# Optimization experiments

Measured on AMD Instinct MI355X. Metric: run time of the kernel, lower is better.

The kernel has to match this reference:

```python
import jax, jax.numpy as jnp
import numpy as np

B, SQ, SK, D, H = 2, 2048, 2048, 1024, 16
DK = D // H


def setup_inputs() -> dict:
    key = jax.random.key(0)
    ks = jax.random.split(key, 16)
    s = 1.0 / np.sqrt(D)
    inp = {
        "query": jax.random.normal(ks[0], (B, SQ, D), jnp.float32),
        "key": jax.random.normal(ks[1], (B, SK, D), jnp.float32),
        "value": jax.random.normal(ks[2], (B, SK, D), jnp.float32),
        "R": jax.random.normal(ks[3], (B, SK, D), jnp.float32),
        "Wq": jax.random.normal(ks[4], (D, D), jnp.float32) * s,
        "bq": jnp.zeros((D,), jnp.float32),
        "Wv": jax.random.normal(ks[5], (D, D), jnp.float32) * s,
        "bv": jnp.zeros((D,), jnp.float32),
        "Wr": jax.random.normal(ks[6], (D, D), jnp.float32) * s,
        "br": jnp.zeros((D,), jnp.float32),
        "W_h": jax.random.normal(ks[7], (H, DK, DK), jnp.float32) * (1.0 / np.sqrt(DK)),
        "Wo": jax.random.normal(ks[8], (D, D), jnp.float32) * s,
        "bo": jnp.zeros((D,), jnp.float32),
    }
    return inp


def _forward(query, key, value, R, Wq, bq, Wv, bv, Wr, br, W_h, Wo, bo):
    scale = 1.0 / np.sqrt(DK)
    # projections (torch Linear: x @ W.T + b)
    Q = (query @ Wq.T + bq).reshape(B, SQ, H, DK).transpose(0, 2, 1, 3)   # (B,H,SQ,DK)
    V = (value @ Wv.T + bv).reshape(B, SK, H, DK).transpose(0, 2, 1, 3)   # (B,H,SK,DK)
    Rp = (R @ Wr.T + br).reshape(B, SK, H, DK).transpose(0, 2, 1, 3)      # (B,H,SK,DK)
    # torch einsum 'hnk,bhn->bhn' sums W_h over its last axis -> elementwise gate
    w_rowsum = W_h.sum(axis=-1)  # (H, DK)

    def step(h, r_t):
        h_new = jnp.tanh(h * w_rowsum + r_t)  # (B,H,DK)
        return h_new, h_new

    h0 = jnp.zeros((B, H, DK), Rp.dtype)
    Rt = Rp.transpose(2, 0, 1, 3)  # (SK,B,H,DK)
    _, Hs = jax.lax.scan(step, h0, Rt)
    Hst = Hs.transpose(1, 2, 0, 3)  # (B,H,SK,DK)

    scores = jnp.einsum('bhqd,bhkd->bhqk', Q, Hst) * scale
    attn = jax.nn.softmax(scores, axis=-1)
    out = jnp.einsum('bhqk,bhkd->bhqd', attn, V)
    out = out.transpose(0, 2, 1, 3).reshape(B, SQ, D)
    return out @ Wo.T + bo


def reference(query, key, value, R, Wq, bq, Wv, bv, Wr, br, W_h, Wo, bo):
    return _forward(query, key, value, R, Wq, bq, Wv, bv, Wr, br, W_h, Wo, bo)
```

## Files before the change

### kernel.cpp

```cpp
#include <hip/hip_runtime.h>
#include <stdint.h>

typedef unsigned short u16;
typedef __attribute__((ext_vector_type(8))) _Float16 h8;
typedef __attribute__((ext_vector_type(2))) __fp16 hp2;
typedef __attribute__((ext_vector_type(4))) float f4;

#define B_ 2
#define SQ_ 2048
#define SK_ 2048
#define D_ 1024
#define H_ 16
#define DK_ 64

#define C_PROG  0
#define CTRL_N  512

__device__ __forceinline__ u16 f2h(float f) {
  union { _Float16 h; u16 u; } v; v.h = (_Float16)f; return v.u;
}
__device__ __forceinline__ unsigned pkrtz(float a, float b) {
  union { hp2 h; unsigned u; } v; v.h = __builtin_amdgcn_cvt_pkrtz(a, b); return v.u;
}
__device__ __forceinline__ float fexp2(float x) {
  float r;
  asm("v_exp_f32 %0, %1" : "=v"(r) : "v"(x));
  return r;
}

typedef const void __attribute__((address_space(1)))* gas1;
typedef void __attribute__((address_space(3)))* las3;
__device__ __forceinline__ void gld16(const void* g, void* l) {
  __builtin_amdgcn_global_load_lds((gas1)g, (las3)l, 16, 0, 0);
}

__device__ __forceinline__ void spin_ge(int* p, int v) {
  if (__hip_atomic_load(p, __ATOMIC_RELAXED, __HIP_MEMORY_SCOPE_AGENT) >= v) return;
  int n = 0;
  for (;;) {
    __builtin_amdgcn_s_sleep(16);
    int x = ((++n & 63) == 0)
                ? __hip_atomic_load(p, __ATOMIC_ACQUIRE, __HIP_MEMORY_SCOPE_AGENT)
                : __hip_atomic_load(p, __ATOMIC_RELAXED, __HIP_MEMORY_SCOPE_AGENT);
    if (x >= v) return;
    if (n > 8192) return;
  }
}

__device__ __forceinline__ void cast8(const float* __restrict__ src,
                                      u16* __restrict__ dst, int i) {
  float4 a = *(const float4*)(src + i);
  float4 b = *(const float4*)(src + i + 4);
  alignas(16) u16 t[8] = {f2h(a.x), f2h(a.y), f2h(a.z), f2h(a.w),
                          f2h(b.x), f2h(b.y), f2h(b.z), f2h(b.w)};
  *(int4*)(dst + i) = *(int4*)t;
}

__global__ void rma_cast_all(const float* __restrict__ xq, const float* __restrict__ xv,
                             const float* __restrict__ xr, const float* __restrict__ wq,
                             const float* __restrict__ wv, const float* __restrict__ wr,
                             const float* __restrict__ wo, u16* __restrict__ oxq,
                             u16* __restrict__ oxv, u16* __restrict__ oxr,
                             u16* __restrict__ owq, u16* __restrict__ owv,
                             u16* __restrict__ owr, u16* __restrict__ owo,
                             int* __restrict__ ctrl) {
  const int b = blockIdx.x;
  if (b == 0) { ctrl[threadIdx.x] = 0; ctrl[256 + threadIdx.x] = 0; }
  const float* src; u16* dst; int bi;
  if (b < 2048)      { src = xq; dst = oxq; bi = b; }
  else if (b < 4096) { src = xv; dst = oxv; bi = b - 2048; }
  else if (b < 6144) { src = xr; dst = oxr; bi = b - 4096; }
  else if (b < 6656) { src = wq; dst = owq; bi = b - 6144; }
  else if (b < 7168) { src = wv; dst = owv; bi = b - 6656; }
  else if (b < 7680) { src = wr; dst = owr; bi = b - 7168; }
  else               { src = wo; dst = owo; bi = b - 7680; }
  cast8(src, dst, (bi * 256 + threadIdx.x) * 8);
}

__device__ __forceinline__ void gemm_mainloop(
    const u16* __restrict__ A, const u16* __restrict__ Bw, int K,
    u16* As, u16* Bs, int m0, int n0, f4 (&acc)[4][4]) {
  const int tid = threadIdx.x;
  const int w = tid >> 6, lane = tid & 63;
  const int quad = lane >> 4, ln = lane & 15;
  const int wm = (w >> 1) * 64, wn = (w & 1) * 64;
  const int c0 = tid, c1 = tid + 256;
  const u16* a0 = A + (size_t)(m0 + (c0 >> 2)) * K + (c0 & 3) * 8;
  const u16* a1 = A + (size_t)(m0 + (c1 >> 2)) * K + (c1 & 3) * 8;
  const u16* b0 = Bw + (size_t)(n0 + (c0 >> 2)) * K + (c0 & 3) * 8;
  const u16* b1 = Bw + (size_t)(n0 + (c1 >> 2)) * K + (c1 & 3) * 8;
  u16* As0 = As + (0 + w * 64) * 8;
  u16* As1 = As + (256 + w * 64) * 8;
  u16* Bs0 = Bs + (0 + w * 64) * 8;
  u16* Bs1 = Bs + (256 + w * 64) * 8;
  for (int kt = 0; kt < K; kt += 32) {
    gld16(a0 + kt, As0);
    gld16(a1 + kt, As1);
    gld16(b0 + kt, Bs0);
    gld16(b1 + kt, Bs1);
    __syncthreads();
    h8 af[4], bf[4];
#pragma unroll
    for (int i = 0; i < 4; i++)
      af[i] = *(const h8*)&As[(wm + i * 16 + ln) * 32 + quad * 8];
#pragma unroll
    for (int i = 0; i < 4; i++)
      bf[i] = *(const h8*)&Bs[(wn + i * 16 + ln) * 32 + quad * 8];
#pragma unroll
    for (int i = 0; i < 4; i++)
#pragma unroll
      for (int j = 0; j < 4; j++)
        acc[i][j] = __builtin_amdgcn_mfma_f32_16x16x32_f16(af[i], bf[j], acc[i][j], 0, 0, 0);
    __syncthreads();
  }
}

__device__ __forceinline__ void gemm_mainloop64(
    const u16* __restrict__ A, const u16* __restrict__ Bw, int K,
    u16* As, u16* Bs, int m0, int n0, f4 (&acc)[2][4]) {
  const int tid = threadIdx.x;
  const int w = tid >> 6, lane = tid & 63;
  const int quad = lane >> 4, ln = lane & 15;
  const int wm = (w >> 1) * 32, wn = (w & 1) * 64;
  const u16* a0 = A + (size_t)(m0 + (tid >> 2)) * K + (tid & 3) * 8;
  const u16* b0 = Bw + (size_t)(n0 + (tid >> 2)) * K + (tid & 3) * 8;
  const u16* b1 = Bw + (size_t)(n0 + ((tid + 256) >> 2)) * K + (tid & 3) * 8;
  u16* As0 = As + (w * 64) * 8;
  u16* Bs0 = Bs + (w * 64) * 8;
  u16* Bs1 = Bs + (256 + w * 64) * 8;
  for (int kt = 0; kt < K; kt += 32) {
    gld16(a0 + kt, As0);
    gld16(b0 + kt, Bs0);
    gld16(b1 + kt, Bs1);
    __syncthreads();
    h8 af[2], bf[4];
#pragma unroll
    for (int i = 0; i < 2; i++)
      af[i] = *(const h8*)&As[(wm + i * 16 + ln) * 32 + quad * 8];
#pragma unroll
    for (int j = 0; j < 4; j++)
      bf[j] = *(const h8*)&Bs[(wn + j * 16 + ln) * 32 + quad * 8];
#pragma unroll
    for (int i = 0; i < 2; i++)
#pragma unroll
      for (int j = 0; j < 4; j++)
        acc[i][j] = __builtin_amdgcn_mfma_f32_16x16x32_f16(af[i], bf[j], acc[i][j], 0, 0, 0);
    __syncthreads();
  }
}

__global__ __launch_bounds__(256, 2)
void rma_proj_gemm(const u16* __restrict__ Xq, const u16* __restrict__ Xv,
                   const u16* __restrict__ Xr, const u16* __restrict__ Wq,
                   const u16* __restrict__ Wv, const u16* __restrict__ Wr,
                   const float* __restrict__ bq, const float* __restrict__ bv,
                   const float* __restrict__ br, u16* __restrict__ Qb,
                   u16* __restrict__ Vt, float* __restrict__ Rp) {
  const int z = blockIdx.z;
  const u16* A = z == 0 ? Xq : (z == 1 ? Xv : Xr);
  const u16* Bw = z == 0 ? Wq : (z == 1 ? Wv : Wr);
  const float* bias = z == 0 ? bq : (z == 1 ? bv : br);
  __shared__ u16 As[128 * 32];
  __shared__ u16 Bs[128 * 32];
  const int m0 = blockIdx.x * 128, n0 = blockIdx.y * 128;
  f4 acc[4][4] = {};
  gemm_mainloop(A, Bw, D_, As, Bs, m0, n0, acc);
  const int tid = threadIdx.x;
  const int w = tid >> 6, lane = tid & 63;
  const int quad = lane >> 4, ln = lane & 15;
  const int wm = (w >> 1) * 64, wn = (w & 1) * 64;
#pragma unroll
  for (int i = 0; i < 4; i++)
#pragma unroll
    for (int j = 0; j < 4; j++) {
      const int colg = n0 + wn + j * 16 + ln;
      const float bb = bias[colg];
      const int h = colg >> 6, d = colg & 63;
      const int row4 = m0 + wm + i * 16 + quad * 4;
      const int b = row4 >> 11, s = row4 & 2047;
      if (z == 1) {
        uint2 pk;
        pk.x = pkrtz(acc[i][j][0] + bb, acc[i][j][1] + bb);
        pk.y = pkrtz(acc[i][j][2] + bb, acc[i][j][3] + bb);
        *(uint2*)&Vt[((size_t)((b * H_ + h) * DK_ + d)) * SK_ + s] = pk;
      } else {
#pragma unroll
        for (int r = 0; r < 4; r++) {
          const float v = acc[i][j][r] + bb;
          const size_t idx = ((size_t)(b * H_ + h) * SK_ + (s + r)) * DK_ + d;
          if (z == 2) Rp[idx] = v;
          else Qb[idx] = f2h(v);
        }
      }
    }
}

#define RB_ 32
__device__ void recur_run(const float* __restrict__ Rp, const float* __restrict__ Wh,
                          u16* __restrict__ Hst, int* ctrl) {
  __builtin_amdgcn_s_setprio(2);
  const int tid = threadIdx.x;
  const int ch = blockIdx.x * 256 + tid;
  const int bh = ch >> 6, d = ch & 63, h = bh & 15;
  const float* wr = Wh + (h * 64 + d) * 64;
  float ws = 0.f;
#pragma unroll
  for (int k = 0; k < 64; k += 4) {
    float4 wv4 = *(const float4*)(wr + k);
    ws += (wv4.x + wv4.y) + (wv4.z + wv4.w);
  }
  const float C2 = 2.885390081777927f;
  const float wsC2 = ws * C2;
  const float Kw = 2.0f * wsC2;
  const size_t base = (size_t)bh * (SK_ * DK_) + d;
  const float* r = Rp + base;
  u16* o = Hst + base;
  int* pg = ctrl + C_PROG + bh * 16;
  float cur[RB_], nxt[RB_];
#pragma unroll
  for (int j = 0; j < RB_; j++) cur[j] = r[(size_t)j * DK_];
  float e = fexp2(cur[0] * C2);
  for (int t0 = 0; t0 < SK_; t0 += RB_) {
    const int t1 = t0 + RB_;
    const int tn = (t1 < SK_) ? t1 : t0;
#pragma unroll
    for (int j = 0; j < RB_; j++) nxt[j] = r[(size_t)(tn + j) * DK_];
#pragma unroll
    for (int j = 0; j < RB_; j++) {
      const float a = e + 1.0f;
      const float bb = __builtin_amdgcn_rcpf(a);
      const float hs = __builtin_fmaf(-2.0f, bb, 1.0f);
      o[(size_t)(t0 + j) * DK_] = f2h(hs);
      const float rn = (j + 1 < RB_) ? cur[j + 1] : nxt[0];
      const float K = __builtin_fmaf(C2, rn, wsC2);
      const float x = __builtin_fmaf(-Kw, bb, K);
      e = fexp2(x);
    }
    if (((t1 & 127) == 0) && (tid & 63) == 0)
      __hip_atomic_store(pg, t1, __ATOMIC_RELEASE, __HIP_MEMORY_SCOPE_AGENT);
#pragma unroll
    for (int j = 0; j < RB_; j++) cur[j] = nxt[j];
  }
  __builtin_amdgcn_s_setprio(0);
}

#define FXM_ 12.0f
__device__ void flash_task(int fidx, const u16* __restrict__ Qb,
                           const u16* __restrict__ Hst, const u16* __restrict__ Vt,
                           u16* __restrict__ Og, u16* smem, int* ctrl) {
  const int tid = threadIdx.x;
  const int w = tid >> 6, lane = tid & 63;
  const int quad = lane >> 4, ln = lane & 15;
  const int bh = fidx >> 4, qtile = fidx & 15;
  const int q0 = qtile * 128 + w * 32;
  u16* Kt = smem;
  u16* Vts = smem + 64 * 72;
  u16* Pw = smem + 2 * 64 * 72 + w * (32 * 72);
  const float scale2 = 0.18033688011112042f;
  const u16* Qg = Qb + (size_t)bh * SQ_ * DK_;
  const u16* Kg = Hst + (size_t)bh * SK_ * DK_;
  const u16* Vg = Vt + (size_t)bh * DK_ * SK_;
  int* pg = ctrl + C_PROG + bh * 16;
  if (tid == 0) spin_ge(pg, 128);
  __syncthreads();
  h8 qf[2][2];
#pragma unroll
  for (int qt = 0; qt < 2; qt++)
#pragma unroll
    for (int c = 0; c < 2; c++)
      qf[qt][c] = *(const h8*)&Qg[(size_t)(q0 + qt * 16 + ln) * DK_ + c * 32 + quad * 8];
  f4 o[4][2] = {};
  float l[2] = {0.f, 0.f};
  const int c0 = tid, c1 = tid + 256;
  const int r0 = c0 >> 3, o0 = (c0 & 7) * 8;
  const int r1 = c1 >> 3, o1 = (c1 & 7) * 8;
  const u16* kg0 = Kg + (size_t)r0 * DK_ + o0;
  const u16* kg1 = Kg + (size_t)r1 * DK_ + o1;
  const u16* vg0 = Vg + (size_t)r0 * SK_ + o0;
  const u16* vg1 = Vg + (size_t)r1 * SK_ + o1;
  u16* kl0 = &Kt[r0 * 72 + o0];
  u16* kl1 = &Kt[r1 * 72 + o1];
  u16* vl0 = &Vts[r0 * 72 + o0];
  u16* vl1 = &Vts[r1 * 72 + o1];
  int4 ks0 = *(const int4*)(kg0);
  int4 ks1 = *(const int4*)(kg1);
  int4 vs0 = *(const int4*)(vg0);
  int4 vs1 = *(const int4*)(vg1);
  int seen = 128;
  for (int kt = 0; kt < SK_; kt += 64) {
    if (tid == 0) {
      const int need = (kt + 128 <= SK_) ? kt + 128 : SK_;
      if (seen < need) { spin_ge(pg, need); seen = need; }
    }
    __syncthreads();
    *(int4*)kl0 = ks0;
    *(int4*)kl1 = ks1;
    *(int4*)vl0 = vs0;
    *(int4*)vl1 = vs1;
    __syncthreads();
    h8 kf[4][2], vf[4][2];
#pragma unroll
    for (int m = 0; m < 4; m++) {
      kf[m][0] = *(const h8*)&Kt[(m * 16 + ln) * 72 + quad * 8];
      kf[m][1] = *(const h8*)&Kt[(m * 16 + ln) * 72 + 32 + quad * 8];
    }
#pragma unroll
    for (int dt = 0; dt < 4; dt++) {
      vf[dt][0] = *(const h8*)&Vts[(dt * 16 + ln) * 72 + quad * 8];
      vf[dt][1] = *(const h8*)&Vts[(dt * 16 + ln) * 72 + 32 + quad * 8];
    }
    const int ktn = (kt + 64 < SK_) ? kt + 64 : 0;
    ks0 = *(const int4*)(kg0 + (size_t)ktn * DK_);
    ks1 = *(const int4*)(kg1 + (size_t)ktn * DK_);
    vs0 = *(const int4*)(vg0 + ktn);
    vs1 = *(const int4*)(vg1 + ktn);
    f4 st[4][2];
#pragma unroll
    for (int m = 0; m < 4; m++)
#pragma unroll
      for (int qt = 0; qt < 2; qt++) {
        f4 t = {0.f, 0.f, 0.f, 0.f};
        t = __builtin_amdgcn_mfma_f32_16x16x32_f16(kf[m][0], qf[qt][0], t, 0, 0, 0);
        t = __builtin_amdgcn_mfma_f32_16x16x32_f16(kf[m][1], qf[qt][1], t, 0, 0, 0);
        st[m][qt] = t;
      }
#pragma unroll
    for (int qt = 0; qt < 2; qt++)
#pragma unroll
      for (int m = 0; m < 4; m++) {
        const float p0 = fexp2(__builtin_fmaf(st[m][qt][0], scale2, -FXM_));
        const float p1 = fexp2(__builtin_fmaf(st[m][qt][1], scale2, -FXM_));
        const float p2 = fexp2(__builtin_fmaf(st[m][qt][2], scale2, -FXM_));
        const float p3 = fexp2(__builtin_fmaf(st[m][qt][3], scale2, -FXM_));
        l[qt] += (p0 + p1) + (p2 + p3);
        uint2 pk;
        pk.x = pkrtz(p0, p1);
        pk.y = pkrtz(p2, p3);
        *(uint2*)&Pw[(qt * 16 + ln) * 72 + m * 16 + quad * 4] = pk;
      }
    asm volatile("" ::: "memory");
#pragma unroll
    for (int c = 0; c < 2; c++) {
      h8 pb0 = *(const h8*)&Pw[(0 + ln) * 72 + c * 32 + quad * 8];
      h8 pb1 = *(const h8*)&Pw[(16 + ln) * 72 + c * 32 + quad * 8];
#pragma unroll
      for (int dt = 0; dt < 4; dt++) {
        o[dt][0] = __builtin_amdgcn_mfma_f32_16x16x32_f16(vf[dt][c], pb0, o[dt][0], 0, 0, 0);
        o[dt][1] = __builtin_amdgcn_mfma_f32_16x16x32_f16(vf[dt][c], pb1, o[dt][1], 0, 0, 0);
      }
    }
  }
  const int b = bh >> 4, h = bh & 15;
#pragma unroll
  for (int qt = 0; qt < 2; qt++) {
    float lq = l[qt];
    lq += __shfl_xor(lq, 16);
    lq += __shfl_xor(lq, 32);
    const float linv = __builtin_amdgcn_rcpf(lq);
    const int q = q0 + qt * 16 + ln;
#pragma unroll
    for (int dt = 0; dt < 4; dt++) {
      uint2 pk;
      pk.x = pkrtz(o[dt][qt][0] * linv, o[dt][qt][1] * linv);
      pk.y = pkrtz(o[dt][qt][2] * linv, o[dt][qt][3] * linv);
      *(uint2*)&Og[((size_t)b * SQ_ + q) * D_ + h * DK_ + dt * 16 + quad * 4] = pk;
    }
  }
}

__global__ __launch_bounds__(256, 2)
void rma_recur_flash(const float* __restrict__ Rp, const float* __restrict__ Wh,
                     u16* __restrict__ Hst, const u16* __restrict__ Qb,
                     const u16* __restrict__ Vt, u16* __restrict__ Og,
                     int* __restrict__ ctrl) {
  __shared__ __align__(16) u16 smem[18432];
  if (blockIdx.x < 8) {
    recur_run(Rp, Wh, Hst, ctrl);
    return;
  }
  flash_task(blockIdx.x - 8, Qb, Hst, Vt, Og, smem, ctrl);
}

__global__ __launch_bounds__(256, 2)
void rma_final_gemm(const u16* __restrict__ Og, const u16* __restrict__ Wo,
                    const float* __restrict__ bo, float* __restrict__ out) {
  __shared__ u16 As[64 * 32];
  __shared__ u16 Bs[128 * 32];
  const int m0 = blockIdx.x * 64, n0 = blockIdx.y * 128;
  f4 acc[2][4] = {};
  gemm_mainloop64(Og, Wo, D_, As, Bs, m0, n0, acc);
  const int tid = threadIdx.x;
  const int w = tid >> 6, lane = tid & 63;
  const int quad = lane >> 4, ln = lane & 15;
  const int wm = (w >> 1) * 32, wn = (w & 1) * 64;
#pragma unroll
  for (int i = 0; i < 2; i++)
#pragma unroll
    for (int j = 0; j < 4; j++) {
      const int colg = n0 + wn + j * 16 + ln;
      const float bb = bo[colg];
#pragma unroll
      for (int r = 0; r < 4; r++) {
        const int rowg = m0 + wm + i * 16 + quad * 4 + r;
        out[(size_t)rowg * D_ + colg] = acc[i][j][r] + bb;
      }
    }
}

extern "C" void kernel_launch(void* const* d_in, const int* in_sizes, int n_in,
                              void* d_out, int out_size, void* d_ws, size_t ws_size,
                              hipStream_t stream) {
  const float* query = (const float*)d_in[0];
  const float* value = (const float*)d_in[2];
  const float* R = (const float*)d_in[3];
  const float* Wq = (const float*)d_in[4];
  const float* bq = (const float*)d_in[5];
  const float* Wv = (const float*)d_in[6];
  const float* bv = (const float*)d_in[7];
  const float* Wr = (const float*)d_in[8];
  const float* br = (const float*)d_in[9];
  const float* W_h = (const float*)d_in[10];
  const float* Wo = (const float*)d_in[11];
  const float* bo = (const float*)d_in[12];
  float* out = (float*)d_out;

  char* ws = (char*)d_ws;
  const size_t MB = 1 << 20;
  u16* Xq = (u16*)(ws + 0 * MB);
  u16* Xv = (u16*)(ws + 8 * MB);
  u16* Xr = (u16*)(ws + 16 * MB);
  u16* Wqb = (u16*)(ws + 24 * MB);
  u16* Wvb = (u16*)(ws + 26 * MB);
  u16* Wrb = (u16*)(ws + 28 * MB);
  u16* Wob = (u16*)(ws + 30 * MB);
  u16* Qb = (u16*)(ws + 32 * MB);
  u16* Vt = (u16*)(ws + 40 * MB);
  float* Rp = (float*)(ws + 48 * MB);
  u16* Hs = (u16*)(ws + 64 * MB);
  u16* Og = (u16*)(ws + 72 * MB);
  int* ctrl = (int*)(ws + 80 * MB);

  rma_cast_all<<<dim3(8192), 256, 0, stream>>>(query, value, R, Wq, Wv, Wr, Wo,
                                               Xq, Xv, Xr, Wqb, Wvb, Wrb, Wob, ctrl);
  rma_proj_gemm<<<dim3(32, 8, 3), 256, 0, stream>>>(Xq, Xv, Xr, Wqb, Wvb, Wrb,
                                                    bq, bv, br, Qb, Vt, Rp);
  rma_recur_flash<<<dim3(520), 256, 0, stream>>>(Rp, W_h, Hs, Qb, Vt, Og, ctrl);
  rma_final_gemm<<<dim3(64, 8), 256, 0, stream>>>(Og, Wob, bo, out);
}
```

Measured before the change: 286.0 us.

## Fuse cast, projections, recurrence, attention and output GEMM into one persistent kernel

Merges the four launches (cast, projection GEMM, recurrence+flash, output GEMM) into a single persistent 520-block kernel coordinated by global atomic counters. The R path is cast and projected first, and the recurrence waits on per-row-tile counters, so it can start before the Q/V projections finish. The output GEMM starts per tile once the matching attention tiles are done. This removes kernel-launch boundaries and lets the serial recurrence overlap the rest, but it relies on all blocks being co-resident and on spin-waits with a timeout fallback, which risks deadlock or reading incomplete data. Launch bounds are raised to 4 blocks per CU.

```diff
diff --git a/kernel.cpp b/kernel.cpp
--- a/kernel.cpp
+++ b/kernel.cpp
@@ -13,8 +13,13 @@
 #define H_ 16
 #define DK_ 64
 
-#define C_PROG  0
-#define CTRL_N  512
+#define C_CASTRW 0
+#define C_CAST   4
+#define C_PROJ   8
+#define C_RDONE  32
+#define C_PROG   64
+#define C_OG     576
+#define CTRL_N   1088
 
 __device__ __forceinline__ u16 f2h(float f) {
   union { _Float16 h; u16 u; } v; v.h = (_Float16)f; return v.u;
@@ -43,8 +48,15 @@
                 ? __hip_atomic_load(p, __ATOMIC_ACQUIRE, __HIP_MEMORY_SCOPE_AGENT)
                 : __hip_atomic_load(p, __ATOMIC_RELAXED, __HIP_MEMORY_SCOPE_AGENT);
     if (x >= v) return;
-    if (n > 8192) return;
-  }
+    if (n > 16384) return;
+  }
+}
+__device__ __forceinline__ void rel_add(int* p, int v) {
+  __hip_atomic_fetch_add(p, v, __ATOMIC_RELEASE, __HIP_MEMORY_SCOPE_AGENT);
+}
+
+__global__ void rma_init(int* __restrict__ ctrl) {
+  for (int k = threadIdx.x; k < CTRL_N; k += 256) ctrl[k] = 0;
 }
 
 __device__ __forceinline__ void cast8(const float* __restrict__ src,
@@ -56,25 +68,23 @@
   *(int4*)(dst + i) = *(int4*)t;
 }
 
-__global__ void rma_cast_all(const float* __restrict__ xq, const float* __restrict__ xv,
-                             const float* __restrict__ xr, const float* __restrict__ wq,
-                             const float* __restrict__ wv, const float* __restrict__ wr,
-                             const float* __restrict__ wo, u16* __restrict__ oxq,
-                             u16* __restrict__ oxv, u16* __restrict__ oxr,
-                             u16* __restrict__ owq, u16* __restrict__ owv,
-                             u16* __restrict__ owr, u16* __restrict__ owo,
-                             int* __restrict__ ctrl) {
-  const int b = blockIdx.x;
-  if (b == 0) { ctrl[threadIdx.x] = 0; ctrl[256 + threadIdx.x] = 0; }
-  const float* src; u16* dst; int bi;
-  if (b < 2048)      { src = xq; dst = oxq; bi = b; }
-  else if (b < 4096) { src = xv; dst = oxv; bi = b - 2048; }
-  else if (b < 6144) { src = xr; dst = oxr; bi = b - 4096; }
-  else if (b < 6656) { src = wq; dst = owq; bi = b - 6144; }
-  else if (b < 7168) { src = wv; dst = owv; bi = b - 6656; }
-  else if (b < 7680) { src = wr; dst = owr; bi = b - 7168; }
-  else               { src = wo; dst = owo; bi = b - 7680; }
-  cast8(src, dst, (bi * 256 + threadIdx.x) * 8);
+__device__ __forceinline__ void cast_unit(
+    int u, int tid, const float* __restrict__ q, const float* __restrict__ v,
+    const float* __restrict__ r, const float* __restrict__ wq,
+    const float* __restrict__ wv, const float* __restrict__ wr,
+    const float* __restrict__ wo, u16* __restrict__ xq, u16* __restrict__ xv,
+    u16* __restrict__ xr, u16* __restrict__ owq, u16* __restrict__ owv,
+    u16* __restrict__ owr, u16* __restrict__ owo) {
+  const float* src; u16* dst; int off;
+  if (u < 256)      { src = r;  dst = xr;  off = u << 14; }
+  else if (u < 320) { src = wr; dst = owr; off = (u - 256) << 14; }
+  else if (u < 576) { src = q;  dst = xq;  off = (u - 320) << 14; }
+  else if (u < 832) { src = v;  dst = xv;  off = (u - 576) << 14; }
+  else if (u < 896) { src = wq; dst = owq; off = (u - 832) << 14; }
+  else if (u < 960) { src = wv; dst = owv; off = (u - 896) << 14; }
+  else              { src = wo; dst = owo; off = (u - 960) << 14; }
+#pragma unroll
+  for (int it = 0; it < 8; it++) cast8(src, dst, off + it * 2048 + tid * 8);
 }
 
 __device__ __forceinline__ void gemm_mainloop(
@@ -149,59 +159,13 @@
   }
 }
 
-__global__ __launch_bounds__(256, 2)
-void rma_proj_gemm(const u16* __restrict__ Xq, const u16* __restrict__ Xv,
-                   const u16* __restrict__ Xr, const u16* __restrict__ Wq,
-                   const u16* __restrict__ Wv, const u16* __restrict__ Wr,
-                   const float* __restrict__ bq, const float* __restrict__ bv,
-                   const float* __restrict__ br, u16* __restrict__ Qb,
-                   u16* __restrict__ Vt, float* __restrict__ Rp) {
-  const int z = blockIdx.z;
-  const u16* A = z == 0 ? Xq : (z == 1 ? Xv : Xr);
-  const u16* Bw = z == 0 ? Wq : (z == 1 ? Wv : Wr);
-  const float* bias = z == 0 ? bq : (z == 1 ? bv : br);
-  __shared__ u16 As[128 * 32];
-  __shared__ u16 Bs[128 * 32];
-  const int m0 = blockIdx.x * 128, n0 = blockIdx.y * 128;
-  f4 acc[4][4] = {};
-  gemm_mainloop(A, Bw, D_, As, Bs, m0, n0, acc);
-  const int tid = threadIdx.x;
-  const int w = tid >> 6, lane = tid & 63;
-  const int quad = lane >> 4, ln = lane & 15;
-  const int wm = (w >> 1) * 64, wn = (w & 1) * 64;
-#pragma unroll
-  for (int i = 0; i < 4; i++)
-#pragma unroll
-    for (int j = 0; j < 4; j++) {
-      const int colg = n0 + wn + j * 16 + ln;
-      const float bb = bias[colg];
-      const int h = colg >> 6, d = colg & 63;
-      const int row4 = m0 + wm + i * 16 + quad * 4;
-      const int b = row4 >> 11, s = row4 & 2047;
-      if (z == 1) {
-        uint2 pk;
-        pk.x = pkrtz(acc[i][j][0] + bb, acc[i][j][1] + bb);
-        pk.y = pkrtz(acc[i][j][2] + bb, acc[i][j][3] + bb);
-        *(uint2*)&Vt[((size_t)((b * H_ + h) * DK_ + d)) * SK_ + s] = pk;
-      } else {
-#pragma unroll
-        for (int r = 0; r < 4; r++) {
-          const float v = acc[i][j][r] + bb;
-          const size_t idx = ((size_t)(b * H_ + h) * SK_ + (s + r)) * DK_ + d;
-          if (z == 2) Rp[idx] = v;
-          else Qb[idx] = f2h(v);
-        }
-      }
-    }
-}
-
 #define RB_ 32
 __device__ void recur_run(const float* __restrict__ Rp, const float* __restrict__ Wh,
                           u16* __restrict__ Hst, int* ctrl) {
   __builtin_amdgcn_s_setprio(2);
   const int tid = threadIdx.x;
   const int ch = blockIdx.x * 256 + tid;
-  const int bh = ch >> 6, d = ch & 63, h = bh & 15;
+  const int bh = ch >> 6, d = ch & 63, h = bh & 15, b = bh >> 4;
   const float* wr = Wh + (h * 64 + d) * 64;
   float ws = 0.f;
 #pragma unroll
@@ -215,13 +179,16 @@
   const size_t base = (size_t)bh * (SK_ * DK_) + d;
   const float* r = Rp + base;
   u16* o = Hst + base;
+  int* rd = ctrl + C_RDONE + b * 16;
   int* pg = ctrl + C_PROG + bh * 16;
+  spin_ge(&rd[0], 8);
   float cur[RB_], nxt[RB_];
 #pragma unroll
   for (int j = 0; j < RB_; j++) cur[j] = r[(size_t)j * DK_];
   float e = fexp2(cur[0] * C2);
   for (int t0 = 0; t0 < SK_; t0 += RB_) {
     const int t1 = t0 + RB_;
+    if (t1 < SK_ && ((t1 & 127) == 0)) spin_ge(&rd[t1 >> 7], 8);
     const int tn = (t1 < SK_) ? t1 : t0;
 #pragma unroll
     for (int j = 0; j < RB_; j++) nxt[j] = r[(size_t)(tn + j) * DK_];
@@ -261,7 +228,7 @@
   const u16* Kg = Hst + (size_t)bh * SK_ * DK_;
   const u16* Vg = Vt + (size_t)bh * DK_ * SK_;
   int* pg = ctrl + C_PROG + bh * 16;
-  if (tid == 0) spin_ge(pg, 128);
+  if (tid == 0) { spin_ge(&ctrl[C_PROJ], 512); spin_ge(pg, 128); }
   __syncthreads();
   h8 qf[2][2];
 #pragma unroll
@@ -368,43 +335,128 @@
   }
 }
 
-__global__ __launch_bounds__(256, 2)
-void rma_recur_flash(const float* __restrict__ Rp, const float* __restrict__ Wh,
-                     u16* __restrict__ Hst, const u16* __restrict__ Qb,
-                     const u16* __restrict__ Vt, u16* __restrict__ Og,
-                     int* __restrict__ ctrl) {
+__global__ __launch_bounds__(256, 4)
+void rma_mega(const float* __restrict__ query, const float* __restrict__ value,
+              const float* __restrict__ R, const float* __restrict__ Wq,
+              const float* __restrict__ Wv, const float* __restrict__ Wr,
+              const float* __restrict__ Wo, u16* __restrict__ Xq,
+              u16* __restrict__ Xv, u16* __restrict__ Xr, u16* __restrict__ Wqb,
+              u16* __restrict__ Wvb, u16* __restrict__ Wrb, u16* __restrict__ Wob,
+              const float* __restrict__ bq, const float* __restrict__ bv,
+              const float* __restrict__ br, const float* __restrict__ bo,
+              const float* __restrict__ Wh, float* __restrict__ Rp,
+              u16* __restrict__ Qb, u16* __restrict__ Vt, u16* __restrict__ Hst,
+              u16* __restrict__ Og, float* __restrict__ out,
+              int* __restrict__ ctrl) {
   __shared__ __align__(16) u16 smem[18432];
+  const int tid = threadIdx.x;
   if (blockIdx.x < 8) {
     recur_run(Rp, Wh, Hst, ctrl);
     return;
   }
-  flash_task(blockIdx.x - 8, Qb, Hst, Vt, Og, smem, ctrl);
-}
-
-__global__ __launch_bounds__(256, 2)
-void rma_final_gemm(const u16* __restrict__ Og, const u16* __restrict__ Wo,
-                    const float* __restrict__ bo, float* __restrict__ out) {
-  __shared__ u16 As[64 * 32];
-  __shared__ u16 Bs[128 * 32];
-  const int m0 = blockIdx.x * 64, n0 = blockIdx.y * 128;
-  f4 acc[2][4] = {};
-  gemm_mainloop64(Og, Wo, D_, As, Bs, m0, n0, acc);
-  const int tid = threadIdx.x;
-  const int w = tid >> 6, lane = tid & 63;
+  const int wk = blockIdx.x - 8;
+  u16* As = smem;
+  u16* Bs = smem + 4096;
+  const int lane = tid & 63, w = tid >> 6;
   const int quad = lane >> 4, ln = lane & 15;
-  const int wm = (w >> 1) * 32, wn = (w & 1) * 64;
-#pragma unroll
-  for (int i = 0; i < 2; i++)
-#pragma unroll
-    for (int j = 0; j < 4; j++) {
-      const int colg = n0 + wn + j * 16 + ln;
-      const float bb = bo[colg];
-#pragma unroll
-      for (int r = 0; r < 4; r++) {
-        const int rowg = m0 + wm + i * 16 + quad * 4 + r;
-        out[(size_t)rowg * D_ + colg] = acc[i][j][r] + bb;
+
+  cast_unit(wk, tid, query, value, R, Wq, Wv, Wr, Wo,
+            Xq, Xv, Xr, Wqb, Wvb, Wrb, Wob);
+  __syncthreads();
+  if (tid == 0 && wk < 320) rel_add(&ctrl[C_CASTRW], 1);
+  cast_unit(wk + 512, tid, query, value, R, Wq, Wv, Wr, Wo,
+            Xq, Xv, Xr, Wqb, Wvb, Wrb, Wob);
+  __syncthreads();
+  if (tid == 0) rel_add(&ctrl[C_CAST], 2);
+
+  if (wk < 256) {
+    if (tid == 0) spin_ge(&ctrl[C_CASTRW], 320);
+    __syncthreads();
+    const int m = wk >> 3, n0 = (wk & 7) << 7, m0 = m << 7;
+    f4 acc[4][4] = {};
+    gemm_mainloop(Xr, Wrb, D_, As, Bs, m0, n0, acc);
+    const int wm = (w >> 1) * 64, wn = (w & 1) * 64;
+#pragma unroll
+    for (int i = 0; i < 4; i++)
+#pragma unroll
+      for (int j = 0; j < 4; j++) {
+        const int colg = n0 + wn + j * 16 + ln;
+        const float bb = br[colg];
+        const int h = colg >> 6, d = colg & 63;
+        const int row4 = m0 + wm + i * 16 + quad * 4;
+        const int b = row4 >> 11, s = row4 & 2047;
+#pragma unroll
+        for (int r2 = 0; r2 < 4; r2++)
+          Rp[((size_t)(b * H_ + h) * SK_ + (s + r2)) * DK_ + d] = acc[i][j][r2] + bb;
       }
-    }
+    __syncthreads();
+    if (tid == 0) rel_add(&ctrl[C_RDONE + m], 1);
+  }
+
+  {
+    if (tid == 0) spin_ge(&ctrl[C_CAST], 1024);
+    __syncthreads();
+    const int z = wk >> 8, t2 = wk & 255;
+    const int m0 = (t2 & 31) << 7, n0 = (t2 >> 5) << 7;
+    const u16* A = z == 0 ? Xq : Xv;
+    const u16* Bw = z == 0 ? Wqb : Wvb;
+    const float* bias = z == 0 ? bq : bv;
+    f4 acc[4][4] = {};
+    gemm_mainloop(A, Bw, D_, As, Bs, m0, n0, acc);
+    const int wm = (w >> 1) * 64, wn = (w & 1) * 64;
+#pragma unroll
+    for (int i = 0; i < 4; i++)
+#pragma unroll
+      for (int j = 0; j < 4; j++) {
+        const int colg = n0 + wn + j * 16 + ln;
+        const float bb = bias[colg];
+        const int h = colg >> 6, d = colg & 63;
+        const int row4 = m0 + wm + i * 16 + quad * 4;
+        const int b = row4 >> 11, s = row4 & 2047;
+        if (z == 1) {
+          uint2 pk;
+          pk.x = pkrtz(acc[i][j][0] + bb, acc[i][j][1] + bb);
+          pk.y = pkrtz(acc[i][j][2] + bb, acc[i][j][3] + bb);
+          *(uint2*)&Vt[((size_t)((b * H_ + h) * DK_ + d)) * SK_ + s] = pk;
+        } else {
+#pragma unroll
+          for (int r2 = 0; r2 < 4; r2++)
+            Qb[((size_t)(b * H_ + h) * SK_ + (s + r2)) * DK_ + d] =
+                f2h(acc[i][j][r2] + bb);
+        }
+      }
+    __syncthreads();
+    if (tid == 0) rel_add(&ctrl[C_PROJ], 1);
+  }
+
+  flash_task(wk, Qb, Hst, Vt, Og, smem, ctrl);
+  __syncthreads();
+  {
+    const int bh = wk >> 4, qq = wk & 15, b = bh >> 4;
+    if (tid == 0) rel_add(&ctrl[C_OG + (b * 16 + qq) * 16], 1);
+  }
+
+  {
+    const int m0 = (wk & 63) * 64, n0 = (wk >> 6) << 7;
+    const int bb_i = m0 >> 11, qq = (m0 & 2047) >> 7;
+    if (tid == 0) spin_ge(&ctrl[C_OG + (bb_i * 16 + qq) * 16], 16);
+    __syncthreads();
+    f4 acc[2][4] = {};
+    gemm_mainloop64(Og, Wob, D_, As, Bs, m0, n0, acc);
+    const int wm = (w >> 1) * 32, wn = (w & 1) * 64;
+#pragma unroll
+    for (int i = 0; i < 2; i++)
+#pragma unroll
+      for (int j = 0; j < 4; j++) {
+        const int colg = n0 + wn + j * 16 + ln;
+        const float bb = bo[colg];
+#pragma unroll
+        for (int r2 = 0; r2 < 4; r2++) {
+          const int rowg = m0 + wm + i * 16 + quad * 4 + r2;
+          out[(size_t)rowg * D_ + colg] = acc[i][j][r2] + bb;
+        }
+      }
+  }
 }
 
 extern "C" void kernel_launch(void* const* d_in, const int* in_sizes, int n_in,
@@ -440,10 +492,9 @@
   u16* Og = (u16*)(ws + 72 * MB);
   int* ctrl = (int*)(ws + 80 * MB);
 
-  rma_cast_all<<<dim3(8192), 256, 0, stream>>>(query, value, R, Wq, Wv, Wr, Wo,
-                                               Xq, Xv, Xr, Wqb, Wvb, Wrb, Wob, ctrl);
-  rma_proj_gemm<<<dim3(32, 8, 3), 256, 0, stream>>>(Xq, Xv, Xr, Wqb, Wvb, Wrb,
-                                                    bq, bv, br, Qb, Vt, Rp);
-  rma_recur_flash<<<dim3(520), 256, 0, stream>>>(Rp, W_h, Hs, Qb, Vt, Og, ctrl);
-  rma_final_gemm<<<dim3(64, 8), 256, 0, stream>>>(Og, Wob, bo, out);
-}
+  rma_init<<<dim3(1), 256, 0, stream>>>(ctrl);
+  rma_mega<<<dim3(520), 256, 0, stream>>>(query, value, R, Wq, Wv, Wr, Wo,
+                                          Xq, Xv, Xr, Wqb, Wvb, Wrb, Wob,
+                                          bq, bv, br, bo, W_h, Rp, Qb, Vt,
+                                          Hs, Og, out, ctrl);
+}
```

After: 609.4 us. +113.0%, slower.

## Fuse fp32-to-fp16 activation cast into projection GEMM A-tile load

Applied to the files above, without the earlier changes.

Drops the separate pass that converted query/value/R to fp16 in workspace. The projection GEMM now loads the fp32 activations directly, converts them in registers and writes them into LDS, while the weights are still pre-cast. This removes a full write and read of the fp16 activation copies. In exchange, the A tile now goes through synchronous register loads instead of async global-to-LDS loads, and each GEMM block re-reads twice as many bytes for A (fp32) across the 8 N-tiles. The spin-wait timeout is also raised.

```diff
diff --git a/kernel.cpp b/kernel.cpp
--- a/kernel.cpp
+++ b/kernel.cpp
@@ -43,7 +43,7 @@
                 ? __hip_atomic_load(p, __ATOMIC_ACQUIRE, __HIP_MEMORY_SCOPE_AGENT)
                 : __hip_atomic_load(p, __ATOMIC_RELAXED, __HIP_MEMORY_SCOPE_AGENT);
     if (x >= v) return;
-    if (n > 8192) return;
+    if (n > 16384) return;
   }
 }
 
@@ -56,48 +56,51 @@
   *(int4*)(dst + i) = *(int4*)t;
 }
 
-__global__ void rma_cast_all(const float* __restrict__ xq, const float* __restrict__ xv,
-                             const float* __restrict__ xr, const float* __restrict__ wq,
-                             const float* __restrict__ wv, const float* __restrict__ wr,
-                             const float* __restrict__ wo, u16* __restrict__ oxq,
-                             u16* __restrict__ oxv, u16* __restrict__ oxr,
-                             u16* __restrict__ owq, u16* __restrict__ owv,
-                             u16* __restrict__ owr, u16* __restrict__ owo,
-                             int* __restrict__ ctrl) {
+__global__ void rma_cast_w(const float* __restrict__ wq, const float* __restrict__ wv,
+                           const float* __restrict__ wr, const float* __restrict__ wo,
+                           u16* __restrict__ owq, u16* __restrict__ owv,
+                           u16* __restrict__ owr, u16* __restrict__ owo,
+                           int* __restrict__ ctrl) {
   const int b = blockIdx.x;
-  if (b == 0) { ctrl[threadIdx.x] = 0; ctrl[256 + threadIdx.x] = 0; }
+  if (b == 0)
+    for (int k = threadIdx.x; k < CTRL_N; k += 256) ctrl[k] = 0;
   const float* src; u16* dst; int bi;
-  if (b < 2048)      { src = xq; dst = oxq; bi = b; }
-  else if (b < 4096) { src = xv; dst = oxv; bi = b - 2048; }
-  else if (b < 6144) { src = xr; dst = oxr; bi = b - 4096; }
-  else if (b < 6656) { src = wq; dst = owq; bi = b - 6144; }
-  else if (b < 7168) { src = wv; dst = owv; bi = b - 6656; }
-  else if (b < 7680) { src = wr; dst = owr; bi = b - 7168; }
-  else               { src = wo; dst = owo; bi = b - 7680; }
+  if (b < 512)        { src = wq; dst = owq; bi = b; }
+  else if (b < 1024)  { src = wv; dst = owv; bi = b - 512; }
+  else if (b < 1536)  { src = wr; dst = owr; bi = b - 1024; }
+  else                { src = wo; dst = owo; bi = b - 1536; }
   cast8(src, dst, (bi * 256 + threadIdx.x) * 8);
 }
 
-__device__ __forceinline__ void gemm_mainloop(
-    const u16* __restrict__ A, const u16* __restrict__ Bw, int K,
+__device__ __forceinline__ void gemm_mainloop_f32a(
+    const float* __restrict__ A, const u16* __restrict__ Bw, int K,
     u16* As, u16* Bs, int m0, int n0, f4 (&acc)[4][4]) {
   const int tid = threadIdx.x;
   const int w = tid >> 6, lane = tid & 63;
   const int quad = lane >> 4, ln = lane & 15;
   const int wm = (w >> 1) * 64, wn = (w & 1) * 64;
   const int c0 = tid, c1 = tid + 256;
-  const u16* a0 = A + (size_t)(m0 + (c0 >> 2)) * K + (c0 & 3) * 8;
-  const u16* a1 = A + (size_t)(m0 + (c1 >> 2)) * K + (c1 & 3) * 8;
+  const float* a0 = A + (size_t)(m0 + (c0 >> 2)) * K + (c0 & 3) * 8;
+  const float* a1 = A + (size_t)(m0 + (c1 >> 2)) * K + (c1 & 3) * 8;
   const u16* b0 = Bw + (size_t)(n0 + (c0 >> 2)) * K + (c0 & 3) * 8;
   const u16* b1 = Bw + (size_t)(n0 + (c1 >> 2)) * K + (c1 & 3) * 8;
-  u16* As0 = As + (0 + w * 64) * 8;
-  u16* As1 = As + (256 + w * 64) * 8;
   u16* Bs0 = Bs + (0 + w * 64) * 8;
   u16* Bs1 = Bs + (256 + w * 64) * 8;
+  u16* Ad0 = As + c0 * 8;
+  u16* Ad1 = As + c1 * 8;
   for (int kt = 0; kt < K; kt += 32) {
-    gld16(a0 + kt, As0);
-    gld16(a1 + kt, As1);
     gld16(b0 + kt, Bs0);
     gld16(b1 + kt, Bs1);
+    float4 x0 = *(const float4*)(a0 + kt);
+    float4 x1 = *(const float4*)(a0 + kt + 4);
+    float4 y0 = *(const float4*)(a1 + kt);
+    float4 y1 = *(const float4*)(a1 + kt + 4);
+    alignas(16) u16 ta[8] = {f2h(x0.x), f2h(x0.y), f2h(x0.z), f2h(x0.w),
+                             f2h(x1.x), f2h(x1.y), f2h(x1.z), f2h(x1.w)};
+    alignas(16) u16 tb[8] = {f2h(y0.x), f2h(y0.y), f2h(y0.z), f2h(y0.w),
+                             f2h(y1.x), f2h(y1.y), f2h(y1.z), f2h(y1.w)};
+    *(int4*)Ad0 = *(int4*)ta;
+    *(int4*)Ad1 = *(int4*)tb;
     __syncthreads();
     h8 af[4], bf[4];
 #pragma unroll
@@ -150,21 +153,21 @@
 }
 
 __global__ __launch_bounds__(256, 2)
-void rma_proj_gemm(const u16* __restrict__ Xq, const u16* __restrict__ Xv,
-                   const u16* __restrict__ Xr, const u16* __restrict__ Wq,
-                   const u16* __restrict__ Wv, const u16* __restrict__ Wr,
-                   const float* __restrict__ bq, const float* __restrict__ bv,
-                   const float* __restrict__ br, u16* __restrict__ Qb,
-                   u16* __restrict__ Vt, float* __restrict__ Rp) {
+void rma_proj3(const float* __restrict__ query, const float* __restrict__ value,
+               const float* __restrict__ R, const u16* __restrict__ Wqb,
+               const u16* __restrict__ Wvb, const u16* __restrict__ Wrb,
+               const float* __restrict__ bq, const float* __restrict__ bv,
+               const float* __restrict__ br, u16* __restrict__ Qb,
+               u16* __restrict__ Vt, float* __restrict__ Rp) {
   const int z = blockIdx.z;
-  const u16* A = z == 0 ? Xq : (z == 1 ? Xv : Xr);
-  const u16* Bw = z == 0 ? Wq : (z == 1 ? Wv : Wr);
+  const float* A = z == 0 ? query : (z == 1 ? value : R);
+  const u16* Bw = z == 0 ? Wqb : (z == 1 ? Wvb : Wrb);
   const float* bias = z == 0 ? bq : (z == 1 ? bv : br);
   __shared__ u16 As[128 * 32];
   __shared__ u16 Bs[128 * 32];
   const int m0 = blockIdx.x * 128, n0 = blockIdx.y * 128;
   f4 acc[4][4] = {};
-  gemm_mainloop(A, Bw, D_, As, Bs, m0, n0, acc);
+  gemm_mainloop_f32a(A, Bw, D_, As, Bs, m0, n0, acc);
   const int tid = threadIdx.x;
   const int w = tid >> 6, lane = tid & 63;
   const int quad = lane >> 4, ln = lane & 15;
@@ -426,9 +429,6 @@
 
   char* ws = (char*)d_ws;
   const size_t MB = 1 << 20;
-  u16* Xq = (u16*)(ws + 0 * MB);
-  u16* Xv = (u16*)(ws + 8 * MB);
-  u16* Xr = (u16*)(ws + 16 * MB);
   u16* Wqb = (u16*)(ws + 24 * MB);
   u16* Wvb = (u16*)(ws + 26 * MB);
   u16* Wrb = (u16*)(ws + 28 * MB);
@@ -440,10 +440,10 @@
   u16* Og = (u16*)(ws + 72 * MB);
   int* ctrl = (int*)(ws + 80 * MB);
 
-  rma_cast_all<<<dim3(8192), 256, 0, stream>>>(query, value, R, Wq, Wv, Wr, Wo,
-                                               Xq, Xv, Xr, Wqb, Wvb, Wrb, Wob, ctrl);
-  rma_proj_gemm<<<dim3(32, 8, 3), 256, 0, stream>>>(Xq, Xv, Xr, Wqb, Wvb, Wrb,
-                                                    bq, bv, br, Qb, Vt, Rp);
+  rma_cast_w<<<dim3(2048), 256, 0, stream>>>(Wq, Wv, Wr, Wo,
+                                             Wqb, Wvb, Wrb, Wob, ctrl);
+  rma_proj3<<<dim3(32, 8, 3), 256, 0, stream>>>(query, value, R, Wqb, Wvb, Wrb,
+                                                bq, bv, br, Qb, Vt, Rp);
   rma_recur_flash<<<dim3(520), 256, 0, stream>>>(Rp, W_h, Hs, Qb, Vt, Og, ctrl);
   rma_final_gemm<<<dim3(64, 8), 256, 0, stream>>>(Og, Wob, bo, out);
 }
```

Result: slower. 302.1 us (+5.6%).
